# Performance work log

Hardware: AMD Instinct MI355X
Metric: run time of the kernel (lower is better)

Reference implementation:

```python
import jax, jax.numpy as jnp
import numpy as np

B, IN, O = 256, 512, 10
STRUCTURES = list(range(32, 257, 32))  # 8 neuron structures
REPS, N_ACT = 4, 4


def _build_hidden_ids():
    ids = []
    i = 0
    # activation-major, then repetition, then structure (matches build_model_ids)
    for _ in range(N_ACT * REPS):
        for s in STRUCTURES:
            ids += [i] * s
            i += 1
    return np.asarray(ids, dtype=np.int32), i


def setup_inputs() -> dict:
    ids, M = _build_hidden_ids()
    H = len(ids)  # 18432
    k = jax.random.split(jax.random.key(0), 5)
    x = jax.random.normal(k[0], (B, IN), dtype=jnp.float32)
    hidden_w = jax.random.normal(k[1], (H, IN), dtype=jnp.float32) / np.sqrt(IN)
    hidden_b = jax.random.normal(k[2], (H,), dtype=jnp.float32) * 0.02
    out_w = jax.random.normal(k[3], (O, H), dtype=jnp.float32) * 0.05
    out_b = jax.random.normal(k[4], (M, O), dtype=jnp.float32) * 0.02
    return {"x": x, "hidden_w": hidden_w, "hidden_b": hidden_b,
            "out_w": out_w, "out_b": out_b,
            "hidden_ids": jnp.asarray(ids)}


_ACTS = [jax.nn.relu, jnp.tanh, jax.nn.sigmoid, lambda t: t]


def reference(x, hidden_w, hidden_b, out_w, out_b, hidden_ids):
    # hidden layer: [B, H]
    h = x @ hidden_w.T + hidden_b
    # per-activation contiguous splits (equal size H // n_act)
    chunks = jnp.split(h, N_ACT, axis=1)
    a = jnp.concatenate([f(c) for f, c in zip(_ACTS, chunks)], axis=1)  # [B, H]
    # per-hidden-neuron contribution to each output unit: [B, H, O]
    contrib = a[:, :, None] * out_w.T[None, :, :]
    M = out_b.shape[0]
    # segment-reduce hidden neurons into their model id: [M, B, O] -> [B, M, O]
    agg = jax.ops.segment_sum(contrib.transpose(1, 0, 2), hidden_ids, num_segments=M)
    return agg.transpose(1, 0, 2) + out_b[None, :, :]
```

## Files before the change

kernel.cpp:

```cpp
#include <hip/hip_runtime.h>
#include <hip/hip_bf16.h>

typedef __bf16 bf16x8 __attribute__((ext_vector_type(8)));
typedef float floatx4 __attribute__((ext_vector_type(4)));

#define BATCH 256
#define INDIM 512
#define ODIM 10
#define HTOT 18432
#define NMODEL 128
#define HTILE 64
#define BTILE 64
#define BK 64
#define LSTRIDE 72
#define ACT_CHUNK 4608
#define NJPG (HTOT / 32)

__device__ __forceinline__ unsigned pk2(float a, float b) {
    unsigned ua = __float_as_uint(a);
    ua = (ua + 0x7fffu + ((ua >> 16) & 1u)) >> 16;
    unsigned ub = __float_as_uint(b);
    ub = (ub + 0x7fffu + ((ub >> 16) & 1u)) >> 16;
    return ua | (ub << 16);
}

__device__ __forceinline__ float apply_act(float h, int aidx) {
    if (aidx == 0) return fmaxf(h, 0.f);
    if (aidx == 1) return 1.f - 2.f / (1.f + __expf(2.f * h));
    if (aidx == 2) return 1.f / (1.f + __expf(-h));
    return h;
}

__global__ __launch_bounds__(256, 4) void mlp_kernel(
    const float* __restrict__ x, const float* __restrict__ hidden_w,
    const float* __restrict__ hidden_b, const float* __restrict__ out_w,
    float* __restrict__ ws)
{
    __shared__ unsigned short xs[BTILE * LSTRIDE];
    __shared__ unsigned short wsx[HTILE * LSTRIDE];
    __shared__ float wtile[ODIM * HTILE];
    __shared__ float btile[HTILE];

    const int tid = threadIdx.x;
    const int bid = blockIdx.x;
    const int r8 = bid & 7, t = bid >> 3;
    const int jb = r8 * 36 + (t >> 2);
    const int bb = t & 3;
    const int j0 = jb * HTILE;
    const int b0 = bb * BTILE;
    const int lane = tid & 63;
    const int wvid = tid >> 6;
    const int r = lane & 15;
    const int g = lane >> 4;

    for (int i = tid; i < ODIM * HTILE; i += 256)
        wtile[i] = out_w[(i >> 6) * HTOT + j0 + (i & 63)];
    if (tid < HTILE) btile[tid] = hidden_b[j0 + tid];

    floatx4 acc[4];
    #pragma unroll
    for (int jt = 0; jt < 4; jt++) acc[jt] = (floatx4)0.f;

    const floatx4* xv  = (const floatx4*)x;
    const floatx4* wv4 = (const floatx4*)hidden_w;

    const int f_row[4] = { (tid + 0)   >> 4, (tid + 256) >> 4,
                           (tid + 512) >> 4, (tid + 768) >> 4 };
    const int f_c4 = tid & 15;

    floatx4 vx[4], vw[4];
    #pragma unroll
    for (int i = 0; i < 4; i++) {
        vx[i] = xv[(size_t)(b0 + f_row[i]) * (INDIM / 4) + f_c4];
        vw[i] = wv4[(size_t)(j0 + f_row[i]) * (INDIM / 4) + f_c4];
    }

    for (int kk = 0; kk < INDIM; kk += BK) {
        #pragma unroll
        for (int i = 0; i < 4; i++) {
            *(uint2*)&xs[f_row[i] * LSTRIDE + f_c4 * 4]  =
                make_uint2(pk2(vx[i][0], vx[i][1]), pk2(vx[i][2], vx[i][3]));
            *(uint2*)&wsx[f_row[i] * LSTRIDE + f_c4 * 4] =
                make_uint2(pk2(vw[i][0], vw[i][1]), pk2(vw[i][2], vw[i][3]));
        }
        __syncthreads();

        if (kk + BK < INDIM) {
            const int kq = (kk + BK) >> 2;
            #pragma unroll
            for (int i = 0; i < 4; i++) {
                vx[i] = xv[(size_t)(b0 + f_row[i]) * (INDIM / 4) + kq + f_c4];
                vw[i] = wv4[(size_t)(j0 + f_row[i]) * (INDIM / 4) + kq + f_c4];
            }
        }

        #pragma unroll
        for (int s = 0; s < 2; s++) {
            bf16x8 bfr = *(const bf16x8*)&xs[(wvid * 16 + r) * LSTRIDE + s * 32 + g * 8];
            #pragma unroll
            for (int jt = 0; jt < 4; jt++) {
                bf16x8 af = *(const bf16x8*)&wsx[(jt * 16 + r) * LSTRIDE + s * 32 + g * 8];
                acc[jt] = __builtin_amdgcn_mfma_f32_16x16x32_bf16(af, bfr, acc[jt], 0, 0, 0);
            }
        }
        __syncthreads();
    }

    const int aidx = j0 / ACT_CHUNK;
    const int b = b0 + wvid * 16 + r;

    #pragma unroll
    for (int jp = 0; jp < 2; jp++) {
        const int jpg = (j0 >> 5) + jp;
        float a[2][4];
        #pragma unroll
        for (int h = 0; h < 2; h++) {
            int jt = jp * 2 + h;
            #pragma unroll
            for (int q = 0; q < 4; q++)
                a[h][q] = apply_act(acc[jt][q] + btile[jt * 16 + g * 4 + q], aidx);
        }
        #pragma unroll
        for (int o = 0; o < ODIM; o++) {
            float p = 0.f;
            #pragma unroll
            for (int h = 0; h < 2; h++) {
                int jt = jp * 2 + h;
                const float* wr = &wtile[o * HTILE + jt * 16 + g * 4];
                p += a[h][0] * wr[0] + a[h][1] * wr[1] + a[h][2] * wr[2] + a[h][3] * wr[3];
            }
            p += __shfl_xor(p, 16, 64);
            p += __shfl_xor(p, 32, 64);
            if (lane < 16)
                ws[((size_t)jpg * ODIM + o) * BATCH + b] = p;
        }
    }
}

__global__ __launch_bounds__(256) void finalize_kernel(
    const float* __restrict__ ws, const float* __restrict__ out_b,
    float* __restrict__ out)
{
    const int mo = blockIdx.x;
    const int m = mo / ODIM, o = mo - m * ODIM;
    const int b = threadIdx.x;
    const int rep = m >> 3, idx = m & 7;
    const int jp0 = rep * 36 + (idx * (idx + 1)) / 2;
    const int cnt = idx + 1;

    float s = out_b[mo];
    for (int c = 0; c < cnt; c++)
        s += ws[((size_t)(jp0 + c) * ODIM + o) * BATCH + b];
    out[((size_t)b * NMODEL + m) * ODIM + o] = s;
}

extern "C" void kernel_launch(void* const* d_in, const int* in_sizes, int n_in,
                              void* d_out, int out_size, void* d_ws, size_t ws_size,
                              hipStream_t stream) {
    const float* x   = (const float*)d_in[0];
    const float* hw  = (const float*)d_in[1];
    const float* hb  = (const float*)d_in[2];
    const float* ow  = (const float*)d_in[3];
    const float* ob  = (const float*)d_in[4];
    float* out = (float*)d_out;
    float* ws  = (float*)d_ws;

    mlp_kernel<<<(HTOT / HTILE) * (BATCH / BTILE), 256, 0, stream>>>(x, hw, hb, ow, ws);
    finalize_kernel<<<NMODEL * ODIM, 256, 0, stream>>>(ws, ob, out);
}
```

Before: 111.8 us.

## Replace workspace+finalize reduction with atomic accumulation into bias-initialized output

Drops the separate finalize kernel and its workspace round trip. A small init kernel now writes the bias into the output, and the main kernel atomically adds each 32-neuron group partial directly into the output slot for its model. The manual bf16 rounding is also replaced with the hardware packed convert instruction. In exchange, atomic contention is added (up to 8 groups per model), the summation order becomes nondeterministic, and the work still needs two launches.

```diff
diff --git a/kernel.cpp b/kernel.cpp
--- a/kernel.cpp
+++ b/kernel.cpp
@@ -17,11 +17,9 @@
 #define NJPG (HTOT / 32)
 
 __device__ __forceinline__ unsigned pk2(float a, float b) {
-    unsigned ua = __float_as_uint(a);
-    ua = (ua + 0x7fffu + ((ua >> 16) & 1u)) >> 16;
-    unsigned ub = __float_as_uint(b);
-    ub = (ub + 0x7fffu + ((ub >> 16) & 1u)) >> 16;
-    return ua | (ub << 16);
+    unsigned r;
+    asm("v_cvt_pk_bf16_f32 %0, %1, %2" : "=v"(r) : "v"(a), "v"(b));
+    return r;
 }
 
 __device__ __forceinline__ float apply_act(float h, int aidx) {
@@ -31,10 +29,18 @@
     return h;
 }
 
+__global__ __launch_bounds__(256) void init_out(
+    const float* __restrict__ out_b, float* __restrict__ out)
+{
+    const int idx = blockIdx.x * 256 + threadIdx.x;
+    const int mo = idx % (NMODEL * ODIM);
+    out[idx] = out_b[mo];
+}
+
 __global__ __launch_bounds__(256, 4) void mlp_kernel(
     const float* __restrict__ x, const float* __restrict__ hidden_w,
     const float* __restrict__ hidden_b, const float* __restrict__ out_w,
-    float* __restrict__ ws)
+    float* __restrict__ out)
 {
     __shared__ unsigned short xs[BTILE * LSTRIDE];
     __shared__ unsigned short wsx[HTILE * LSTRIDE];
@@ -112,6 +118,12 @@
     #pragma unroll
     for (int jp = 0; jp < 2; jp++) {
         const int jpg = (j0 >> 5) + jp;
+        const int rep = jpg / 36;
+        const int w36 = jpg - rep * 36;
+        int sidx = 0;
+        while (w36 >= ((sidx + 1) * (sidx + 2)) / 2) sidx++;
+        const int m = rep * 8 + sidx;
+
         float a[2][4];
         #pragma unroll
         for (int h = 0; h < 2; h++) {
@@ -132,26 +144,9 @@
             p += __shfl_xor(p, 16, 64);
             p += __shfl_xor(p, 32, 64);
             if (lane < 16)
-                ws[((size_t)jpg * ODIM + o) * BATCH + b] = p;
+                atomicAdd(&out[((size_t)b * NMODEL + m) * ODIM + o], p);
         }
     }
-}
-
-__global__ __launch_bounds__(256) void finalize_kernel(
-    const float* __restrict__ ws, const float* __restrict__ out_b,
-    float* __restrict__ out)
-{
-    const int mo = blockIdx.x;
-    const int m = mo / ODIM, o = mo - m * ODIM;
-    const int b = threadIdx.x;
-    const int rep = m >> 3, idx = m & 7;
-    const int jp0 = rep * 36 + (idx * (idx + 1)) / 2;
-    const int cnt = idx + 1;
-
-    float s = out_b[mo];
-    for (int c = 0; c < cnt; c++)
-        s += ws[((size_t)(jp0 + c) * ODIM + o) * BATCH + b];
-    out[((size_t)b * NMODEL + m) * ODIM + o] = s;
 }
 
 extern "C" void kernel_launch(void* const* d_in, const int* in_sizes, int n_in,
@@ -163,8 +158,8 @@
     const float* ow  = (const float*)d_in[3];
     const float* ob  = (const float*)d_in[4];
     float* out = (float*)d_out;
-    float* ws  = (float*)d_ws;
+    (void)d_ws; (void)ws_size;
 
-    mlp_kernel<<<(HTOT / HTILE) * (BATCH / BTILE), 256, 0, stream>>>(x, hw, hb, ow, ws);
-    finalize_kernel<<<NMODEL * ODIM, 256, 0, stream>>>(ws, ob, out);
+    init_out<<<(BATCH * NMODEL * ODIM) / 256, 256, 0, stream>>>(ob, out);
+    mlp_kernel<<<(HTOT / HTILE) * (BATCH / BTILE), 256, 0, stream>>>(x, hw, hb, ow, out);
 }
```

After: 176.7 us. +58.1%, slower.
